# Performance work log

Measured on AMD Instinct MI355X. Metric: run time of the kernel, lower is better.

## Reference

```python
import jax, jax.numpy as jnp
import numpy as np

D_MODEL = 1024
N_EXPERTS = 4
TOP_K = 32


def setup_inputs() -> dict:
    key = jax.random.key(0)
    k1, k2, k3, k4 = jax.random.split(key, 4)
    b, t, d = 2, 2048, D_MODEL
    n_lts = 8192
    h = jax.random.normal(k1, (b, t, d), dtype=jnp.float32)
    lts = jax.random.normal(k2, (1, n_lts, d), dtype=jnp.float32)
    # router: nn.Linear(d_model, n_experts)
    lim = 1.0 / np.sqrt(d)
    W_router = jax.random.uniform(k3, (N_EXPERTS, d), minval=-lim, maxval=lim, dtype=jnp.float32)
    b_router = jax.random.uniform(k4, (N_EXPERTS,), minval=-lim, maxval=lim, dtype=jnp.float32)
    return {"h": h, "lts": lts, "W_router": W_router, "b_router": b_router}


def reference(h, lts, W_router, b_router):
    b, t, d = h.shape
    n_lts = lts.shape[1]
    top_k = TOP_K
    n_experts = N_EXPERTS

    # router (eval mode: no noise)
    logits = jnp.einsum('btd,ed->bte', h, W_router) + b_router  # (b,t,E)
    expert_weights = jax.nn.softmax(logits, axis=-1)
    expert_idx = jnp.argmax(expert_weights, axis=-1)            # (b,t) int

    entries_per_expert = n_lts // n_experts
    offsets = jnp.minimum(expert_idx * entries_per_expert, n_lts - top_k)  # (b,t)
    indices = offsets[..., None] + jnp.arange(top_k)            # (b,t,k)
    indices = jnp.minimum(indices, n_lts - 1)

    # gather memory slices: lts broadcast over batch -> (b,t,k,d)
    selected = jnp.take(lts[0], indices, axis=0)

    # small attention of each token over its top_k memory entries
    scores = jnp.einsum('btd,btkd->btk', h, selected) / jnp.sqrt(jnp.asarray(d, h.dtype))
    attn = jax.nn.softmax(scores, axis=-1)
    result = jnp.einsum('btk,btkd->btd', attn, selected)
    return result, expert_weights
```

## Files before the change

kernel.cpp:

```cpp
#include <hip/hip_runtime.h>
#include <hip/hip_fp16.h>
#include <math.h>

constexpr int D    = 1024;
constexpr int NEXP = 4;
constexpr int EPP  = 2048;

using pk_t = decltype(__builtin_amdgcn_cvt_pkrtz(0.f, 0.f));
typedef _Float16 f16x8 __attribute__((ext_vector_type(8)));
typedef float    f32x4 __attribute__((ext_vector_type(4)));

__device__ __forceinline__ unsigned pk2(float a, float b) {
    return __builtin_bit_cast(unsigned, __builtin_amdgcn_cvt_pkrtz(a, b));
}

__global__ __launch_bounds__(1024) void prep_kernel(
    const float* __restrict__ lts, _Float16* __restrict__ lts16,
    _Float16* __restrict__ ltsT)
{
    const int e = blockIdx.x >> 2, part = blockIdx.x & 3;
    const int tid = threadIdx.x;
    __shared__ _Float16 s[8 * 1024];

    const float4* src = reinterpret_cast<const float4*>(lts + ((size_t)e * EPP + part * 8) * D);
    #pragma unroll
    for (int i = 0; i < 2; ++i) {
        const int f = tid + i * 1024;
        const float4 v = src[f];
        *reinterpret_cast<uint2*>(s + f * 4) = make_uint2(pk2(v.x, v.y), pk2(v.z, v.w));
    }
    __syncthreads();

    const uint4* s4 = reinterpret_cast<const uint4*>(s);
    uint4* d4 = reinterpret_cast<uint4*>(lts16 + ((size_t)e * 32 + part * 8) * D);
    d4[tid] = s4[tid];

    _Float16 tmp[8];
    #pragma unroll
    for (int k = 0; k < 8; ++k) tmp[k] = s[k * 1024 + tid];
    *reinterpret_cast<uint4*>(ltsT + (size_t)e * 32768 + (size_t)tid * 32 + part * 8) =
        *reinterpret_cast<const uint4*>(tmp);
}

__global__ __launch_bounds__(256) void fused_kernel(
    const float* __restrict__ h,
    const _Float16* __restrict__ lts16,
    const _Float16* __restrict__ ltsT,
    const float* __restrict__ Wr, const float* __restrict__ br,
    float* __restrict__ out_res, float* __restrict__ out_ew, int ntok)
{
    const int tid  = threadIdx.x;
    const int wid  = tid >> 6;
    const int lane = tid & 63;
    const int base = blockIdx.x * 16;

    __shared__ __align__(16) unsigned char h_lds[16 * 2048];
    __shared__ __align__(16) unsigned char p_lds[16 * 256];
    __shared__ int experts[16];

    *reinterpret_cast<uint4*>(p_lds + tid * 16) = make_uint4(0, 0, 0, 0);

    {
        const int r = tid >> 4, c = tid & 15;
        int tok = base + r; if (tok > ntok - 1) tok = ntok - 1;
        const float4* src = reinterpret_cast<const float4*>(h + (size_t)tok * D);
        #pragma unroll
        for (int i = 0; i < 8; ++i) {
            const int g = c + 16 * i;
            const float4 a = src[2 * g];
            const float4 b = src[2 * g + 1];
            uint4 u;
            u.x = pk2(a.x, a.y); u.y = pk2(a.z, a.w);
            u.z = pk2(b.x, b.y); u.w = pk2(b.z, b.w);
            *reinterpret_cast<uint4*>(h_lds + r * 2048 + ((g ^ (r & 7)) << 4)) = u;
        }
    }

    {
        const float4* h4 = reinterpret_cast<const float4*>(h);
        const float4* w4 = reinterpret_cast<const float4*>(Wr);
        float4 wf[NEXP][4];
        #pragma unroll
        for (int e = 0; e < NEXP; ++e)
            #pragma unroll
            for (int i = 0; i < 4; ++i)
                wf[e][i] = w4[e * 256 + lane + 64 * i];
        const float bb0 = br[0], bb1 = br[1], bb2 = br[2], bb3 = br[3];

        #pragma unroll
        for (int t = 0; t < 4; ++t) {
            const int tok = base + wid * 4 + t;
            if (tok < ntok) {
                float acc[NEXP] = {0.f, 0.f, 0.f, 0.f};
                #pragma unroll
                for (int i = 0; i < 4; ++i) {
                    const float4 a = h4[(size_t)tok * 256 + lane + 64 * i];
                    #pragma unroll
                    for (int e = 0; e < NEXP; ++e)
                        acc[e] += a.x * wf[e][i].x + a.y * wf[e][i].y
                                + a.z * wf[e][i].z + a.w * wf[e][i].w;
                }
                #pragma unroll
                for (int m = 1; m < 64; m <<= 1)
                    #pragma unroll
                    for (int e = 0; e < NEXP; ++e) acc[e] += __shfl_xor(acc[e], m);
                const float l0 = acc[0] + bb0, l1 = acc[1] + bb1,
                            l2 = acc[2] + bb2, l3 = acc[3] + bb3;
                const float lm = fmaxf(fmaxf(l0, l1), fmaxf(l2, l3));
                const float e0 = __expf(l0 - lm), e1 = __expf(l1 - lm),
                            e2 = __expf(l2 - lm), e3 = __expf(l3 - lm);
                const float einv = 1.f / (e0 + e1 + e2 + e3);
                if (lane < NEXP) {
                    const float ev = (lane == 0) ? e0 : (lane == 1) ? e1 : (lane == 2) ? e2 : e3;
                    out_ew[(size_t)tok * NEXP + lane] = ev * einv;
                }
                int bi = 0; float bv = l0;
                if (l1 > bv) { bv = l1; bi = 1; }
                if (l2 > bv) { bv = l2; bi = 2; }
                if (l3 > bv) { bv = l3; bi = 3; }
                if (lane == 0) experts[wid * 4 + t] = bi;
            } else if (lane == 0) experts[wid * 4 + t] = 0;
        }
    }
    __syncthreads();

    const int rA = lane & 15, g4 = lane >> 4;

    f32x4 s0 = {0.f, 0.f, 0.f, 0.f}, s1 = {0.f, 0.f, 0.f, 0.f};
    {
        const _Float16* b0p = lts16 + (size_t)(wid * 32 + rA) * D + g4 * 8;
        const _Float16* b1p = b0p + 16 * D;
        #pragma unroll
        for (int kc = 0; kc < 32; ++kc) {
            const f16x8 a  = *reinterpret_cast<const f16x8*>(
                h_lds + rA * 2048 + ((((kc << 2) | g4) ^ (rA & 7)) << 4));
            const f16x8 b0 = *reinterpret_cast<const f16x8*>(b0p + kc * 32);
            const f16x8 b1 = *reinterpret_cast<const f16x8*>(b1p + kc * 32);
            s0 = __builtin_amdgcn_mfma_f32_16x16x32_f16(a, b0, s0, 0, 0, 0);
            s1 = __builtin_amdgcn_mfma_f32_16x16x32_f16(a, b1, s1, 0, 0, 0);
        }
    }

    constexpr float inv32 = 1.f / 32.f;
    #pragma unroll
    for (int r = 0; r < 4; ++r) {
        const int tr = g4 * 4 + r;
        if (experts[tr] == wid) {
            float mx = fmaxf(s0[r], s1[r]);
            #pragma unroll
            for (int m = 1; m < 16; m <<= 1) mx = fmaxf(mx, __shfl_xor(mx, m));
            const float e0 = __expf((s0[r] - mx) * inv32);
            const float e1 = __expf((s1[r] - mx) * inv32);
            float sm = e0 + e1;
            #pragma unroll
            for (int m = 1; m < 16; m <<= 1) sm += __shfl_xor(sm, m);
            const float is = 1.f / sm;
            const int G0 = (wid * 4 + (rA >> 3)) ^ (tr & 7);
            const int G1 = (wid * 4 + 2 + (rA >> 3)) ^ (tr & 7);
            *reinterpret_cast<_Float16*>(p_lds + tr * 256 + G0 * 16 + (rA & 7) * 2) = (_Float16)(e0 * is);
            *reinterpret_cast<_Float16*>(p_lds + tr * 256 + G1 * 16 + (rA & 7) * 2) = (_Float16)(e1 * is);
        }
    }
    __syncthreads();

    f16x8 pa[4];
    #pragma unroll
    for (int kc = 0; kc < 4; ++kc)
        pa[kc] = *reinterpret_cast<const f16x8*>(
            p_lds + rA * 256 + ((((kc << 2) | g4) ^ (rA & 7)) << 4));

    int toks[4]; bool tv[4];
    #pragma unroll
    for (int r = 0; r < 4; ++r) { toks[r] = base + g4 * 4 + r; tv[r] = toks[r] < ntok; }

    #pragma unroll
    for (int i = 0; i < 16; ++i) {
        const int dimc = wid * 256 + i * 16 + rA;
        f32x4 o = {0.f, 0.f, 0.f, 0.f};
        #pragma unroll
        for (int kc = 0; kc < 4; ++kc) {
            const f16x8 bk = *reinterpret_cast<const f16x8*>(
                ltsT + ((size_t)kc << 15) + (size_t)dimc * 32 + g4 * 8);
            o = __builtin_amdgcn_mfma_f32_16x16x32_f16(pa[kc], bk, o, 0, 0, 0);
        }
        #pragma unroll
        for (int r = 0; r < 4; ++r)
            if (tv[r]) out_res[(size_t)toks[r] * D + dimc] = o[r];
    }
}

extern "C" void kernel_launch(void* const* d_in, const int* in_sizes, int n_in,
                              void* d_out, int out_size, void* d_ws, size_t ws_size,
                              hipStream_t stream) {
    const float* h   = (const float*)d_in[0];
    const float* lts = (const float*)d_in[1];
    const float* Wr  = (const float*)d_in[2];
    const float* br  = (const float*)d_in[3];

    const int ntok = in_sizes[0] / D;
    float* out_res = (float*)d_out;
    float* out_ew  = out_res + (size_t)ntok * D;

    _Float16* lts16 = (_Float16*)d_ws;
    _Float16* ltsT  = lts16 + (size_t)128 * D;

    prep_kernel<<<16, 1024, 0, stream>>>(lts, lts16, ltsT);
    fused_kernel<<<(ntok + 15) / 16, 256, 0, stream>>>(h, lts16, ltsT, Wr, br,
                                                       out_res, out_ew, ntok);
}
```

Before: 40.90 us.

## Split fused kernel into separate QK/softmax and PV kernels for more parallelism

The single fused kernel is split into a QK kernel and a PV kernel. The QK kernel handles 8 tokens per block, doing routing, scores and softmax, and writes the probabilities and expert index to workspace. The PV kernel splits the output dimension four ways across blocks. The prep kernel also moves to 64 blocks of 256 threads. The aim is more blocks for better occupancy and less serial per-block work, at the cost of an extra launch and a global round trip for the probabilities. The QK MFMA now uses only 8 of 16 A rows, duplicating rows, so half its compute is wasted.

```diff
diff --git a/kernel.cpp b/kernel.cpp
--- a/kernel.cpp
+++ b/kernel.cpp
@@ -6,7 +6,6 @@
 constexpr int NEXP = 4;
 constexpr int EPP  = 2048;
 
-using pk_t = decltype(__builtin_amdgcn_cvt_pkrtz(0.f, 0.f));
 typedef _Float16 f16x8 __attribute__((ext_vector_type(8)));
 typedef float    f32x4 __attribute__((ext_vector_type(4)));
 
@@ -14,65 +13,63 @@
     return __builtin_bit_cast(unsigned, __builtin_amdgcn_cvt_pkrtz(a, b));
 }
 
-__global__ __launch_bounds__(1024) void prep_kernel(
+__global__ __launch_bounds__(256) void prep_kernel(
     const float* __restrict__ lts, _Float16* __restrict__ lts16,
     _Float16* __restrict__ ltsT)
 {
-    const int e = blockIdx.x >> 2, part = blockIdx.x & 3;
+    const int e = blockIdx.x >> 4, part = (blockIdx.x >> 2) & 3, dc = blockIdx.x & 3;
     const int tid = threadIdx.x;
-    __shared__ _Float16 s[8 * 1024];
-
-    const float4* src = reinterpret_cast<const float4*>(lts + ((size_t)e * EPP + part * 8) * D);
+    __shared__ __align__(16) _Float16 s[8][256];
+
+    const float4* src = reinterpret_cast<const float4*>(lts);
     #pragma unroll
     for (int i = 0; i < 2; ++i) {
-        const int f = tid + i * 1024;
-        const float4 v = src[f];
-        *reinterpret_cast<uint2*>(s + f * 4) = make_uint2(pk2(v.x, v.y), pk2(v.z, v.w));
+        const int f = tid + 256 * i;
+        const int r = f >> 6, c4 = f & 63;
+        const float4 v = src[(size_t)(e * EPP + part * 8 + r) * 256 + dc * 64 + c4];
+        *reinterpret_cast<uint2*>(&s[r][c4 * 4]) = make_uint2(pk2(v.x, v.y), pk2(v.z, v.w));
     }
     __syncthreads();
 
-    const uint4* s4 = reinterpret_cast<const uint4*>(s);
-    uint4* d4 = reinterpret_cast<uint4*>(lts16 + ((size_t)e * 32 + part * 8) * D);
-    d4[tid] = s4[tid];
-
-    _Float16 tmp[8];
-    #pragma unroll
-    for (int k = 0; k < 8; ++k) tmp[k] = s[k * 1024 + tid];
-    *reinterpret_cast<uint4*>(ltsT + (size_t)e * 32768 + (size_t)tid * 32 + part * 8) =
-        *reinterpret_cast<const uint4*>(tmp);
-}
-
-__global__ __launch_bounds__(256) void fused_kernel(
-    const float* __restrict__ h,
-    const _Float16* __restrict__ lts16,
-    const _Float16* __restrict__ ltsT,
+    {
+        const int r = tid >> 5, c = tid & 31;
+        *reinterpret_cast<uint4*>(lts16 + (size_t)(e * 32 + part * 8 + r) * D + dc * 256 + c * 8) =
+            *reinterpret_cast<const uint4*>(&s[r][c * 8]);
+    }
+    {
+        _Float16 tmp[8];
+        #pragma unroll
+        for (int k = 0; k < 8; ++k) tmp[k] = s[k][tid];
+        *reinterpret_cast<uint4*>(ltsT + ((size_t)e << 15) + (size_t)(dc * 256 + tid) * 32 + part * 8) =
+            *reinterpret_cast<const uint4*>(tmp);
+    }
+}
+
+__global__ __launch_bounds__(256) void qk_kernel(
+    const float* __restrict__ h, const _Float16* __restrict__ lts16,
     const float* __restrict__ Wr, const float* __restrict__ br,
-    float* __restrict__ out_res, float* __restrict__ out_ew, int ntok)
+    float* __restrict__ out_ew, _Float16* __restrict__ P32,
+    int* __restrict__ eidx, int ntok)
 {
-    const int tid  = threadIdx.x;
-    const int wid  = tid >> 6;
-    const int lane = tid & 63;
-    const int base = blockIdx.x * 16;
-
-    __shared__ __align__(16) unsigned char h_lds[16 * 2048];
-    __shared__ __align__(16) unsigned char p_lds[16 * 256];
-    __shared__ int experts[16];
-
-    *reinterpret_cast<uint4*>(p_lds + tid * 16) = make_uint4(0, 0, 0, 0);
-
-    {
-        const int r = tid >> 4, c = tid & 15;
+    const int tid = threadIdx.x, wid = tid >> 6, lane = tid & 63;
+    const int base = blockIdx.x * 8;
+
+    __shared__ __align__(16) unsigned char h_lds[8 * 2048];
+    __shared__ int experts[8];
+
+    {
+        const int r = tid >> 5, c = tid & 31;
         int tok = base + r; if (tok > ntok - 1) tok = ntok - 1;
         const float4* src = reinterpret_cast<const float4*>(h + (size_t)tok * D);
         #pragma unroll
-        for (int i = 0; i < 8; ++i) {
-            const int g = c + 16 * i;
+        for (int i = 0; i < 4; ++i) {
+            const int g = c + 32 * i;
             const float4 a = src[2 * g];
             const float4 b = src[2 * g + 1];
             uint4 u;
             u.x = pk2(a.x, a.y); u.y = pk2(a.z, a.w);
             u.z = pk2(b.x, b.y); u.w = pk2(b.z, b.w);
-            *reinterpret_cast<uint4*>(h_lds + r * 2048 + ((g ^ (r & 7)) << 4)) = u;
+            *reinterpret_cast<uint4*>(h_lds + r * 2048 + ((g ^ r) << 4)) = u;
         }
     }
 
@@ -88,8 +85,8 @@
         const float bb0 = br[0], bb1 = br[1], bb2 = br[2], bb3 = br[3];
 
         #pragma unroll
-        for (int t = 0; t < 4; ++t) {
-            const int tok = base + wid * 4 + t;
+        for (int t = 0; t < 2; ++t) {
+            const int tok = base + wid * 2 + t;
             if (tok < ntok) {
                 float acc[NEXP] = {0.f, 0.f, 0.f, 0.f};
                 #pragma unroll
@@ -118,34 +115,32 @@
                 if (l1 > bv) { bv = l1; bi = 1; }
                 if (l2 > bv) { bv = l2; bi = 2; }
                 if (l3 > bv) { bv = l3; bi = 3; }
-                if (lane == 0) experts[wid * 4 + t] = bi;
-            } else if (lane == 0) experts[wid * 4 + t] = 0;
+                if (lane == 0) experts[wid * 2 + t] = bi;
+            } else if (lane == 0) experts[wid * 2 + t] = 0;
         }
     }
     __syncthreads();
 
-    const int rA = lane & 15, g4 = lane >> 4;
+    const int rA = lane & 15, g4 = lane >> 4, arow = rA & 7;
 
     f32x4 s0 = {0.f, 0.f, 0.f, 0.f}, s1 = {0.f, 0.f, 0.f, 0.f};
-    {
-        const _Float16* b0p = lts16 + (size_t)(wid * 32 + rA) * D + g4 * 8;
-        const _Float16* b1p = b0p + 16 * D;
-        #pragma unroll
-        for (int kc = 0; kc < 32; ++kc) {
-            const f16x8 a  = *reinterpret_cast<const f16x8*>(
-                h_lds + rA * 2048 + ((((kc << 2) | g4) ^ (rA & 7)) << 4));
-            const f16x8 b0 = *reinterpret_cast<const f16x8*>(b0p + kc * 32);
-            const f16x8 b1 = *reinterpret_cast<const f16x8*>(b1p + kc * 32);
-            s0 = __builtin_amdgcn_mfma_f32_16x16x32_f16(a, b0, s0, 0, 0, 0);
-            s1 = __builtin_amdgcn_mfma_f32_16x16x32_f16(a, b1, s1, 0, 0, 0);
-        }
+    const _Float16* b0p = lts16 + (size_t)(wid * 32 + rA) * D + g4 * 8;
+    const _Float16* b1p = b0p + 16 * D;
+    #pragma unroll
+    for (int kc = 0; kc < 32; ++kc) {
+        const f16x8 a = *reinterpret_cast<const f16x8*>(
+            h_lds + arow * 2048 + ((((kc << 2) | g4) ^ arow) << 4));
+        const f16x8 b0 = *reinterpret_cast<const f16x8*>(b0p + kc * 32);
+        const f16x8 b1 = *reinterpret_cast<const f16x8*>(b1p + kc * 32);
+        s0 = __builtin_amdgcn_mfma_f32_16x16x32_f16(a, b0, s0, 0, 0, 0);
+        s1 = __builtin_amdgcn_mfma_f32_16x16x32_f16(a, b1, s1, 0, 0, 0);
     }
 
     constexpr float inv32 = 1.f / 32.f;
     #pragma unroll
     for (int r = 0; r < 4; ++r) {
         const int tr = g4 * 4 + r;
-        if (experts[tr] == wid) {
+        if (tr < 8 && base + tr < ntok && experts[tr] == wid) {
             float mx = fmaxf(s0[r], s1[r]);
             #pragma unroll
             for (int m = 1; m < 16; m <<= 1) mx = fmaxf(mx, __shfl_xor(mx, m));
@@ -155,27 +150,49 @@
             #pragma unroll
             for (int m = 1; m < 16; m <<= 1) sm += __shfl_xor(sm, m);
             const float is = 1.f / sm;
-            const int G0 = (wid * 4 + (rA >> 3)) ^ (tr & 7);
-            const int G1 = (wid * 4 + 2 + (rA >> 3)) ^ (tr & 7);
-            *reinterpret_cast<_Float16*>(p_lds + tr * 256 + G0 * 16 + (rA & 7) * 2) = (_Float16)(e0 * is);
-            *reinterpret_cast<_Float16*>(p_lds + tr * 256 + G1 * 16 + (rA & 7) * 2) = (_Float16)(e1 * is);
-        }
+            const int tok2 = base + tr;
+            P32[(size_t)tok2 * 32 + rA]      = (_Float16)(e0 * is);
+            P32[(size_t)tok2 * 32 + rA + 16] = (_Float16)(e1 * is);
+            if (rA == 0) eidx[tok2] = wid;
+        }
+    }
+}
+
+__global__ __launch_bounds__(256) void pv_kernel(
+    const _Float16* __restrict__ P32, const int* __restrict__ eidx,
+    const _Float16* __restrict__ ltsT, float* __restrict__ out_res, int ntok)
+{
+    const int tile = blockIdx.x >> 2, q = blockIdx.x & 3;
+    const int tid = threadIdx.x, wid = tid >> 6, lane = tid & 63;
+    __shared__ __align__(16) unsigned char p_lds[16 * 256];
+
+    {
+        const int r = tid >> 4, c = tid & 15;
+        const int tok = tile * 16 + r;
+        uint4 v = make_uint4(0, 0, 0, 0);
+        if (tok < ntok) {
+            const int ex = eidx[tok];
+            if ((c >> 2) == ex)
+                v = *reinterpret_cast<const uint4*>(P32 + (size_t)tok * 32 + (c & 3) * 8);
+        }
+        *reinterpret_cast<uint4*>(p_lds + r * 256 + ((c ^ (r & 7)) << 4)) = v;
     }
     __syncthreads();
 
+    const int rA = lane & 15, g4 = lane >> 4;
     f16x8 pa[4];
     #pragma unroll
     for (int kc = 0; kc < 4; ++kc)
         pa[kc] = *reinterpret_cast<const f16x8*>(
             p_lds + rA * 256 + ((((kc << 2) | g4) ^ (rA & 7)) << 4));
 
-    int toks[4]; bool tv[4];
-    #pragma unroll
-    for (int r = 0; r < 4; ++r) { toks[r] = base + g4 * 4 + r; tv[r] = toks[r] < ntok; }
-
-    #pragma unroll
-    for (int i = 0; i < 16; ++i) {
-        const int dimc = wid * 256 + i * 16 + rA;
+    int toks[4];
+    #pragma unroll
+    for (int r = 0; r < 4; ++r) toks[r] = tile * 16 + g4 * 4 + r;
+
+    #pragma unroll
+    for (int i = 0; i < 4; ++i) {
+        const int dimc = q * 256 + wid * 64 + i * 16 + rA;
         f32x4 o = {0.f, 0.f, 0.f, 0.f};
         #pragma unroll
         for (int kc = 0; kc < 4; ++kc) {
@@ -185,7 +202,7 @@
         }
         #pragma unroll
         for (int r = 0; r < 4; ++r)
-            if (tv[r]) out_res[(size_t)toks[r] * D + dimc] = o[r];
+            if (toks[r] < ntok) out_res[(size_t)toks[r] * D + dimc] = o[r];
     }
 }
 
@@ -203,8 +220,10 @@
 
     _Float16* lts16 = (_Float16*)d_ws;
     _Float16* ltsT  = lts16 + (size_t)128 * D;
-
-    prep_kernel<<<16, 1024, 0, stream>>>(lts, lts16, ltsT);
-    fused_kernel<<<(ntok + 15) / 16, 256, 0, stream>>>(h, lts16, ltsT, Wr, br,
-                                                       out_res, out_ew, ntok);
-}
+    _Float16* P32   = ltsT + (size_t)NEXP * D * 32;
+    int*      eidx  = (int*)(P32 + (size_t)ntok * 32);
+
+    prep_kernel<<<64, 256, 0, stream>>>(lts, lts16, ltsT);
+    qk_kernel<<<(ntok + 7) / 8, 256, 0, stream>>>(h, lts16, Wr, br, out_ew, P32, eidx, ntok);
+    pv_kernel<<<((ntok + 15) / 16) * 4, 256, 0, stream>>>(P32, eidx, ltsT, out_res, ntok);
+}
```

Result: faster. 39.86 us (-2.5%).
